# Kernel optimization log

Hardware: AMD Instinct MI355X
Metric: run time of the kernel (lower is better)

Reference implementation:

```python
import jax, jax.numpy as jnp
import numpy as np

H_DIM = 1024
N_HEADS = 16
HEAD_D = H_DIM // N_HEADS  # 64


def setup_inputs() -> dict:
    key = jax.random.key(0)
    ks = jax.random.split(key, 10)
    B, T, C = 2, 2048, H_DIM
    init = 1.0 / np.sqrt(C)  # lecun_normal-scale stand-in
    src = jax.random.normal(ks[0], (B, T, C), dtype=jnp.float32)
    mask = jnp.ones((B, T), dtype=jnp.float32)  # unused when causal
    Wq = jax.random.normal(ks[1], (C, H_DIM), dtype=jnp.float32) * init
    Wk = jax.random.normal(ks[2], (C, H_DIM), dtype=jnp.float32) * init
    Wv = jax.random.normal(ks[3], (C, H_DIM), dtype=jnp.float32) * init
    Wo = jax.random.normal(ks[4], (H_DIM, H_DIM), dtype=jnp.float32) * init
    bq = jnp.zeros((H_DIM,), jnp.float32)
    bk = jnp.zeros((H_DIM,), jnp.float32)
    bv = jnp.zeros((H_DIM,), jnp.float32)
    bo = jnp.zeros((H_DIM,), jnp.float32)
    return {"src": src, "mask": mask, "Wq": Wq, "bq": bq, "Wk": Wk, "bk": bk,
            "Wv": Wv, "bv": bv, "Wo": Wo, "bo": bo}


def reference(src, mask, Wq, bq, Wk, bk, Wv, bv, Wo, bo):
    # MaskedCausalAttention forward, deterministic=True (dropout = identity),
    # use_causal_mask=True.
    B, T, C = src.shape
    N, D = N_HEADS, HEAD_D
    # q,k,v: [B, N, T, D]
    q = (src @ Wq + bq).reshape(B, T, N, D).transpose(0, 2, 1, 3)
    k = (src @ Wk + bk).reshape(B, T, N, D).transpose(0, 2, 1, 3)
    v = (src @ Wv + bv).reshape(B, T, N, D).transpose(0, 2, 1, 3)
    # scores: [B, N, T, T]
    scores = jnp.einsum('bntd,bnsd->bnts', q, k) / jnp.sqrt(jnp.float32(D))
    causal = jnp.tril(jnp.ones((T, T), dtype=bool))[None, None]
    scores = jnp.where(causal, scores, -jnp.inf)
    probs = jax.nn.softmax(scores, axis=-1)
    attn = jnp.einsum('bnts,bnsd->bntd', probs, v)  # [B, N, T, D]
    attn = attn.transpose(0, 2, 1, 3).reshape(B, T, N * D)
    return attn @ Wo + bo
```

## Files before the change

### kernel.cpp

```cpp
#include <hip/hip_runtime.h>
#include <hip/hip_bf16.h>

typedef __hip_bfloat16 bf16;
typedef __attribute__((ext_vector_type(8))) short short8;
typedef __attribute__((ext_vector_type(4))) float f32x4;

#define BATCH 2
#define SEQ   2048
#define HDIM  1024
#define NHEAD 16
#define DHEAD 64
#define MROWS (BATCH*SEQ)

#define QSCALE 0.18033688f
#define EXP2F(x) __builtin_amdgcn_exp2f(x)

static __device__ __forceinline__ short f2bs(float x) {
    __hip_bfloat16 h = (__hip_bfloat16)x;
    return *reinterpret_cast<short*>(&h);
}
static __device__ __forceinline__ unsigned int pk2(float a, float b) {
    __hip_bfloat162 h = __float22bfloat162_rn(make_float2(a, b));
    return *reinterpret_cast<unsigned int*>(&h);
}

static __device__ __forceinline__ void gload16(const void* g, void* l) {
    __builtin_amdgcn_global_load_lds(
        (const __attribute__((address_space(1))) unsigned int*)g,
        (__attribute__((address_space(3))) unsigned int*)l, 16, 0, 0);
}

__global__ __launch_bounds__(256) void prep1(const float* __restrict__ src,
        const float* __restrict__ Wq, const float* __restrict__ Wk,
        const float* __restrict__ Wv, const float* __restrict__ Wo,
        short* __restrict__ Sb, short* __restrict__ WT,
        short* __restrict__ WoT)
{
    __shared__ float t[64][65];
    const int bx = blockIdx.x, tid = threadIdx.x;
    if (bx < 4096) {
        int i = bx * 256 + tid;
        float4 v = ((const float4*)src)[i];
        ushort4 o;
        o.x = (unsigned short)f2bs(v.x);
        o.y = (unsigned short)f2bs(v.y);
        o.z = (unsigned short)f2bs(v.z);
        o.w = (unsigned short)f2bs(v.w);
        ((ushort4*)Sb)[i] = o;
        return;
    }
    const int tb = bx - 4096;
    const int wsel = tb >> 8;
    const float* W = (wsel == 0) ? Wq : (wsel == 1) ? Wk : (wsel == 2) ? Wv : Wo;
    short* dst = (wsel < 3) ? WT : WoT;
    const int roff = (wsel < 3) ? wsel * 1024 : 0;
    const int t8 = tb & 255;
    const int n0 = (t8 & 15) * 64, k0 = (t8 >> 4) * 64;
#pragma unroll
    for (int i = 0; i < 16; i++) {
        int idx = tid + i * 256, r = idx >> 6, c = idx & 63;
        t[r][c] = W[(size_t)(k0 + r) * HDIM + n0 + c];
    }
    __syncthreads();
#pragma unroll
    for (int i = 0; i < 16; i++) {
        int idx = tid + i * 256, c = idx >> 6, r = idx & 63;
        dst[(size_t)(roff + n0 + c) * HDIM + k0 + r] = f2bs(t[r][c]);
    }
}

__global__ __launch_bounds__(512, 2) void gemm_qkv(const short* __restrict__ A,
        const short* __restrict__ Bt,
        const float* __restrict__ bq, const float* __restrict__ bk,
        const float* __restrict__ bv,
        short* __restrict__ Qout, short* __restrict__ Kout,
        short* __restrict__ Vtout)
{
    __shared__ short SM[2][32768];
    const int tid = threadIdx.x, lane = tid & 63, w = tid >> 6;
    const int quad = lane >> 4, l15 = lane & 15;
    const int m0 = blockIdx.y * 256, n0 = blockIdx.x * 256;
    const int wr = w >> 1, wc = w & 1;

    const short* gp[4][2];
    int lo[4][2];
#pragma unroll
    for (int g = 0; g < 4; g++)
#pragma unroll
        for (int i = 0; i < 2; i++) {
            if (g < 2) {
                int u = g * 16 + w * 2 + i;
                gp[g][i] = A + (size_t)(m0 + (u >> 1) * 16 + l15) * HDIM
                             + (u & 1) * 32 + quad * 8;
                lo[g][i] = u * 512;
            } else {
                int j = w * 2 + i;
                int v = (g == 2 ? 0 : 8) + j + (j >= 8 ? 8 : 0);
                gp[g][i] = Bt + (size_t)(n0 + (v >> 1) * 16 + l15) * HDIM
                              + (v & 1) * 32 + quad * 8;
                lo[g][i] = 16384 + v * 512;
            }
        }

    f32x4 acc[4][8];
#pragma unroll
    for (int i = 0; i < 4; i++)
#pragma unroll
        for (int j = 0; j < 8; j++) acc[i][j] = (f32x4){0.f, 0.f, 0.f, 0.f};

#pragma unroll
    for (int g = 0; g < 4; g++)
#pragma unroll
        for (int i = 0; i < 2; i++) { gload16(gp[g][i], &SM[0][lo[g][i]]); gp[g][i] += 64; }
    asm volatile("s_waitcnt vmcnt(2)" ::: "memory");
    __builtin_amdgcn_s_barrier();

    short8 af[4][2];
    for (int t = 0; t < 16; ++t) {
        const short* Tb = SM[t & 1];
        short* Sn = SM[(t + 1) & 1];
#pragma unroll
        for (int p = 0; p < 4; ++p) {
            if (p == 0) {
#pragma unroll
                for (int mi = 0; mi < 4; mi++)
#pragma unroll
                    for (int kh = 0; kh < 2; kh++)
                        af[mi][kh] = *(const short8*)
                            &Tb[((wr * 4 + mi) * 2 + kh) * 512 + lane * 8];
            }
            short8 bfp[2][2];
#pragma unroll
            for (int n2 = 0; n2 < 2; n2++)
#pragma unroll
                for (int kh = 0; kh < 2; kh++)
                    bfp[n2][kh] = *(const short8*)
                        &Tb[16384 + ((wc * 8 + p * 2 + n2) * 2 + kh) * 512 + lane * 8];

            if (t < 15) {
                gload16(gp[p][0], Sn + lo[p][0]); gp[p][0] += 64;
                gload16(gp[p][1], Sn + lo[p][1]); gp[p][1] += 64;
                if (p == 1) asm volatile("s_waitcnt vmcnt(4)" ::: "memory");
                if (p == 3) asm volatile("s_waitcnt vmcnt(2)" ::: "memory");
            } else {
                if (p == 1) asm volatile("s_waitcnt vmcnt(0)" ::: "memory");
            }
            __builtin_amdgcn_s_barrier();
            asm volatile("s_waitcnt lgkmcnt(0)" ::: "memory");
            __builtin_amdgcn_s_setprio(1);
#pragma unroll
            for (int n2 = 0; n2 < 2; n2++)
#pragma unroll
                for (int mi = 0; mi < 4; mi++)
#pragma unroll
                    for (int kh = 0; kh < 2; kh++)
                        acc[mi][p * 2 + n2] = __builtin_amdgcn_mfma_f32_16x16x32_bf16(
                            af[mi][kh], bfp[n2][kh], acc[mi][p * 2 + n2], 0, 0, 0);
            __builtin_amdgcn_s_setprio(0);
            __builtin_amdgcn_s_barrier();
        }
    }

    const int region = blockIdx.x >> 2;
    if (region < 2) {
        const float* bias = region ? bk : bq;
        const float oscale = region ? 1.0f : QSCALE;
        short* C = region ? Kout : Qout;
#pragma unroll
        for (int mi = 0; mi < 4; mi++) {
            int mB = m0 + wr * 64 + mi * 16 + quad * 4;
#pragma unroll
            for (int ni = 0; ni < 8; ni++) {
                int nl = (n0 + (wc * 8 + ni) * 16 + l15) & 1023;
                float bb = bias[nl];
#pragma unroll
                for (int r = 0; r < 4; r++)
                    C[(size_t)(mB + r) * HDIM + nl] =
                        f2bs((acc[mi][ni][r] + bb) * oscale);
            }
        }
    } else {
#pragma unroll
        for (int mi = 0; mi < 4; mi++) {
            int mB = m0 + wr * 64 + mi * 16 + quad * 4;
            int bb = mB >> 11, tt = mB & 2047;
#pragma unroll
            for (int ni = 0; ni < 8; ni++) {
                int n = n0 + (wc * 8 + ni) * 16 + l15;
                int h = (n >> 6) & 15, d = n & 63;
                float bvv = bv[n & 1023];
                size_t base = ((size_t)((bb * NHEAD + h) * DHEAD + d)) * SEQ + tt;
                ushort4 pk;
                pk.x = (unsigned short)f2bs(acc[mi][ni][0] + bvv);
                pk.y = (unsigned short)f2bs(acc[mi][ni][1] + bvv);
                pk.z = (unsigned short)f2bs(acc[mi][ni][2] + bvv);
                pk.w = (unsigned short)f2bs(acc[mi][ni][3] + bvv);
                *(ushort4*)(Vtout + base) = pk;
            }
        }
    }
}

__global__ __launch_bounds__(256) void attn_mfma(const short* __restrict__ Qb,
        const short* __restrict__ Kb, const short* __restrict__ Vt,
        short* __restrict__ Ab)
{
    __shared__ short SMEM[29184];
    const int tid = threadIdx.x, lane = tid & 63, w = tid >> 6;
    const int quad = lane >> 4, l15 = lane & 15;
    const int L = blockIdx.x;

    const int pair = (L & 7) + 8 * ((L >> 3) & 3);
    const int strip = 31 - (L >> 5);
    const int b = pair >> 4, head = pair & 15;

    const short* Kbh = Kb + (size_t)b * SEQ * HDIM + head * DHEAD;
    const short* Vth = Vt + (size_t)(b * NHEAD + head) * DHEAD * SEQ;
    short* Pw = SMEM + 24576 + w * 1152;

    const int qbase = strip * 64;
    const int qr = qbase + w * 16 + l15;

    const short* qptr = Qb + (size_t)(b * SEQ + qr) * HDIM + head * DHEAD + quad * 8;
    short8 bq0 = *(const short8*)qptr;
    short8 bq1 = *(const short8*)(qptr + 32);

    const short* gp[4];
    int stp[4], ldo[4];
#pragma unroll
    for (int i = 0; i < 4; i++) {
        int u = w * 4 + i;
        if (u < 8) {
            int t = u >> 1, h = u & 1;
            gp[i] = Kbh + (size_t)(t * 16 + l15) * HDIM + h * 32 + quad * 8;
            stp[i] = 64 * HDIM;
        } else {
            int c = u - 8, dt = c >> 1, kh = c & 1;
            gp[i] = Vth + (size_t)(dt * 16 + l15) * SEQ + kh * 32 + quad * 8;
            stp[i] = 64;
        }
        ldo[i] = u * 512;
    }

    f32x4 o[4];
#pragma unroll
    for (int dt = 0; dt < 4; dt++) o[dt] = (f32x4){0.f, 0.f, 0.f, 0.f};
    float psum = 0.f;

#pragma unroll
    for (int i = 0; i < 4; i++) { gload16(gp[i], &SMEM[ldo[i]]); gp[i] += stp[i]; }
    if (strip >= 1) {
#pragma unroll
        for (int i = 0; i < 4; i++) { gload16(gp[i], &SMEM[8192 + ldo[i]]); gp[i] += stp[i]; }
    }

    for (int it = 0; it <= strip; ++it) {
        short* Ks = &SMEM[(it % 3) * 8192];
        short* Vs = Ks + 4096;

        if (it + 2 <= strip) {
            short* nb = &SMEM[((it + 2) % 3) * 8192];
#pragma unroll
            for (int i = 0; i < 4; i++) { gload16(gp[i], nb + ldo[i]); gp[i] += stp[i]; }
            asm volatile("s_waitcnt vmcnt(8)" ::: "memory");
        } else if (it + 1 <= strip) {
            asm volatile("s_waitcnt vmcnt(4)" ::: "memory");
        } else {
            asm volatile("s_waitcnt vmcnt(0)" ::: "memory");
        }
        __builtin_amdgcn_s_barrier();
        const int s0 = it * 64;
        f32x4 sv[4];
        __builtin_amdgcn_s_setprio(1);
#pragma unroll
        for (int t = 0; t < 4; t++) {
            sv[t] = (f32x4){0.f, 0.f, 0.f, 0.f};
            short8 k0 = *(const short8*)&Ks[(t * 2) * 512 + lane * 8];
            short8 k1 = *(const short8*)&Ks[(t * 2 + 1) * 512 + lane * 8];
            sv[t] = __builtin_amdgcn_mfma_f32_16x16x32_bf16(k0, bq0, sv[t], 0, 0, 0);
            sv[t] = __builtin_amdgcn_mfma_f32_16x16x32_bf16(k1, bq1, sv[t], 0, 0, 0);
        }
        __builtin_amdgcn_s_setprio(0);

        float p[16];
        if (it == strip) {
#pragma unroll
            for (int t = 0; t < 4; t++)
#pragma unroll
                for (int r = 0; r < 4; r++) {
                    int key = s0 + t * 16 + quad * 4 + r;
                    p[t * 4 + r] = (key <= qr) ? EXP2F(sv[t][r]) : 0.f;
                }
        } else {
#pragma unroll
            for (int t = 0; t < 4; t++)
#pragma unroll
                for (int r = 0; r < 4; r++)
                    p[t * 4 + r] = EXP2F(sv[t][r]);
        }
#pragma unroll
        for (int i = 0; i < 16; i++) psum += p[i];

#pragma unroll
        for (int t = 0; t < 4; t++) {
            uint2 u2;
            u2.x = pk2(p[t * 4],     p[t * 4 + 1]);
            u2.y = pk2(p[t * 4 + 2], p[t * 4 + 3]);
            *(uint2*)&Pw[l15 * 72 + t * 16 + quad * 4] = u2;
        }
        short8 bp0 = *(const short8*)&Pw[l15 * 72 + quad * 8];
        short8 bp1 = *(const short8*)&Pw[l15 * 72 + 32 + quad * 8];

        __builtin_amdgcn_s_setprio(1);
#pragma unroll
        for (int dt = 0; dt < 4; dt++) {
            short8 av0 = *(const short8*)&Vs[(dt * 2) * 512 + lane * 8];
            short8 av1 = *(const short8*)&Vs[(dt * 2 + 1) * 512 + lane * 8];
            o[dt] = __builtin_amdgcn_mfma_f32_16x16x32_bf16(av0, bp0, o[dt], 0, 0, 0);
            o[dt] = __builtin_amdgcn_mfma_f32_16x16x32_bf16(av1, bp1, o[dt], 0, 0, 0);
        }
        __builtin_amdgcn_s_setprio(0);
        __builtin_amdgcn_s_barrier();
    }

    float lrow = psum + __shfl_xor(psum, 16);
    lrow += __shfl_xor(lrow, 32);
    const float inv = 1.f / lrow;

    const size_t obase = (size_t)(b * SEQ + qr) * HDIM + head * DHEAD;
#pragma unroll
    for (int dt = 0; dt < 4; dt++) {
        uint2 u2;
        u2.x = pk2(o[dt][0] * inv, o[dt][1] * inv);
        u2.y = pk2(o[dt][2] * inv, o[dt][3] * inv);
        *(uint2*)&Ab[obase + dt * 16 + quad * 4] = u2;
    }
}

__global__ __launch_bounds__(256) void gemm_o(const short* __restrict__ A,
        const short* __restrict__ Bt, const float* __restrict__ bo,
        float* __restrict__ Out)
{
    __shared__ short SM[3 * 6144];
    const int tid = threadIdx.x, lane = tid & 63, w = tid >> 6;
    const int quad = lane >> 4, l15 = lane & 15;
    const int m0 = blockIdx.y * 64, n0 = blockIdx.x * 128;
    const int wr = w >> 1, wc = w & 1;

    const short* gsrc[3];
    short* ldst[3];
#pragma unroll
    for (int i = 0; i < 3; i++) {
        int u = w * 3 + i;
        if (u < 4) {
            gsrc[i] = A + (size_t)(m0 + u * 16 + l15) * HDIM + quad * 8;
            ldst[i] = &SM[u * 512];
        } else {
            int v = u - 4;
            gsrc[i] = Bt + (size_t)(n0 + v * 16 + l15) * HDIM + quad * 8;
            ldst[i] = &SM[2048 + v * 512];
        }
    }

    f32x4 acc[2][4];
#pragma unroll
    for (int i = 0; i < 2; i++)
#pragma unroll
        for (int j = 0; j < 4; j++) acc[i][j] = (f32x4){0.f, 0.f, 0.f, 0.f};

#pragma unroll
    for (int i = 0; i < 3; i++) { gload16(gsrc[i], ldst[i]); gsrc[i] += 32; }
#pragma unroll
    for (int i = 0; i < 3; i++) { gload16(gsrc[i], ldst[i] + 6144); gsrc[i] += 32; }

    for (int kk = 0; kk < 32; ++kk) {
        if (kk < 30) {
            const int nb = ((kk + 2) % 3) * 6144;
#pragma unroll
            for (int i = 0; i < 3; i++) { gload16(gsrc[i], ldst[i] + nb); gsrc[i] += 32; }
            asm volatile("s_waitcnt vmcnt(6)" ::: "memory");
        } else if (kk == 30) {
            asm volatile("s_waitcnt vmcnt(3)" ::: "memory");
        } else {
            asm volatile("s_waitcnt vmcnt(0)" ::: "memory");
        }
        __builtin_amdgcn_s_barrier();

        const short* Asb = &SM[(kk % 3) * 6144];
        const short* Bsb = Asb + 2048;
        short8 af[2], bfr[4];
#pragma unroll
        for (int mi = 0; mi < 2; mi++)
            af[mi] = *(const short8*)&Asb[(wr * 2 + mi) * 512 + lane * 8];
#pragma unroll
        for (int ni = 0; ni < 4; ni++)
            bfr[ni] = *(const short8*)&Bsb[(wc * 4 + ni) * 512 + lane * 8];
#pragma unroll
        for (int mi = 0; mi < 2; mi++)
#pragma unroll
            for (int ni = 0; ni < 4; ni++)
                acc[mi][ni] = __builtin_amdgcn_mfma_f32_16x16x32_bf16(
                                  af[mi], bfr[ni], acc[mi][ni], 0, 0, 0);
        __builtin_amdgcn_s_barrier();
    }

#pragma unroll
    for (int mi = 0; mi < 2; mi++) {
        int mB = m0 + (wr * 2 + mi) * 16 + quad * 4;
#pragma unroll
        for (int ni = 0; ni < 4; ni++) {
            int n = n0 + (wc * 4 + ni) * 16 + l15;
            float bb = bo[n];
#pragma unroll
            for (int r = 0; r < 4; r++)
                Out[(size_t)(mB + r) * HDIM + n] = acc[mi][ni][r] + bb;
        }
    }
}

extern "C" void kernel_launch(void* const* d_in, const int* in_sizes, int n_in,
                              void* d_out, int out_size, void* d_ws, size_t ws_size,
                              hipStream_t stream)
{
    const float* src = (const float*)d_in[0];
    const float* Wq = (const float*)d_in[2];
    const float* bq = (const float*)d_in[3];
    const float* Wk = (const float*)d_in[4];
    const float* bk = (const float*)d_in[5];
    const float* Wv = (const float*)d_in[6];
    const float* bv = (const float*)d_in[7];
    const float* Wo = (const float*)d_in[8];
    const float* bo = (const float*)d_in[9];
    float* out = (float*)d_out;

    short* Sb   = (short*)d_ws;
    short* Qb   = Sb + (size_t)MROWS * HDIM;
    short* Kb   = Qb + (size_t)MROWS * HDIM;
    short* Vt   = Kb + (size_t)MROWS * HDIM;
    short* WoT  = Vt + (size_t)MROWS * HDIM;
    short* WT   = (short*)d_out;
    short* Ab   = Qb;

    prep1<<<dim3(4096 + 1024), dim3(256), 0, stream>>>(src, Wq, Wk, Wv, Wo, Sb, WT, WoT);

    gemm_qkv<<<dim3(12, 16), dim3(512), 0, stream>>>(Sb, WT, bq, bk, bv, Qb, Kb, Vt);

    attn_mfma<<<dim3(1024), dim3(256), 0, stream>>>(Qb, Kb, Vt, Ab);

    gemm_o<<<dim3(8, 64), dim3(256), 0, stream>>>(Ab, WoT, bo, out);
}
```

Measured before the change: 206.7 us.

## Switch attention and output GEMM to double buffering with larger K tiles

The attention kernel drops from triple to double buffering of K/V tiles, cutting shared memory from about 58KB to 42KB. That should allow more blocks per CU at the cost of a shallower prefetch. The output-projection GEMM now uses a K step of 64 with two buffers instead of 32 with three, halving the iteration and barrier count per block. An explicit lgkmcnt wait after the barrier in the QKV GEMM is also removed, leaving the compiler to insert LDS waits.

After: 203.7 us. No clear change (-1.4%).

```diff
diff --git a/kernel.cpp b/kernel.cpp
--- a/kernel.cpp
+++ b/kernel.cpp
@@ -146,7 +146,6 @@
                 if (p == 1) asm volatile("s_waitcnt vmcnt(0)" ::: "memory");
             }
             __builtin_amdgcn_s_barrier();
-            asm volatile("s_waitcnt lgkmcnt(0)" ::: "memory");
             __builtin_amdgcn_s_setprio(1);
 #pragma unroll
             for (int n2 = 0; n2 < 2; n2++)
@@ -205,7 +204,7 @@
         const short* __restrict__ Kb, const short* __restrict__ Vt,
         short* __restrict__ Ab)
 {
-    __shared__ short SMEM[29184];
+    __shared__ short SMEM[20992];
     const int tid = threadIdx.x, lane = tid & 63, w = tid >> 6;
     const int quad = lane >> 4, l15 = lane & 15;
     const int L = blockIdx.x;
@@ -216,7 +215,7 @@
 
     const short* Kbh = Kb + (size_t)b * SEQ * HDIM + head * DHEAD;
     const short* Vth = Vt + (size_t)(b * NHEAD + head) * DHEAD * SEQ;
-    short* Pw = SMEM + 24576 + w * 1152;
+    short* Pw = SMEM + 16384 + w * 1152;
 
     const int qbase = strip * 64;
     const int qr = qbase + w * 16 + l15;
@@ -249,21 +248,16 @@
 
 #pragma unroll
     for (int i = 0; i < 4; i++) { gload16(gp[i], &SMEM[ldo[i]]); gp[i] += stp[i]; }
-    if (strip >= 1) {
-#pragma unroll
-        for (int i = 0; i < 4; i++) { gload16(gp[i], &SMEM[8192 + ldo[i]]); gp[i] += stp[i]; }
-    }
 
     for (int it = 0; it <= strip; ++it) {
-        short* Ks = &SMEM[(it % 3) * 8192];
+        const int cur = it & 1;
+        short* Ks = &SMEM[cur * 8192];
         short* Vs = Ks + 4096;
 
-        if (it + 2 <= strip) {
-            short* nb = &SMEM[((it + 2) % 3) * 8192];
+        if (it < strip) {
+            short* nb = &SMEM[(cur ^ 1) * 8192];
 #pragma unroll
             for (int i = 0; i < 4; i++) { gload16(gp[i], nb + ldo[i]); gp[i] += stp[i]; }
-            asm volatile("s_waitcnt vmcnt(8)" ::: "memory");
-        } else if (it + 1 <= strip) {
             asm volatile("s_waitcnt vmcnt(4)" ::: "memory");
         } else {
             asm volatile("s_waitcnt vmcnt(0)" ::: "memory");
@@ -341,24 +335,25 @@
         const short* __restrict__ Bt, const float* __restrict__ bo,
         float* __restrict__ Out)
 {
-    __shared__ short SM[3 * 6144];
+    __shared__ short SM[2 * 12288];
     const int tid = threadIdx.x, lane = tid & 63, w = tid >> 6;
     const int quad = lane >> 4, l15 = lane & 15;
     const int m0 = blockIdx.y * 64, n0 = blockIdx.x * 128;
     const int wr = w >> 1, wc = w & 1;
 
-    const short* gsrc[3];
-    short* ldst[3];
-#pragma unroll
-    for (int i = 0; i < 3; i++) {
-        int u = w * 3 + i;
-        if (u < 4) {
-            gsrc[i] = A + (size_t)(m0 + u * 16 + l15) * HDIM + quad * 8;
+    const short* gsrc[6];
+    short* ldst[6];
+#pragma unroll
+    for (int i = 0; i < 6; i++) {
+        int u = w * 6 + i;
+        if (u < 8) {
+            int mi = u >> 1, kh = u & 1;
+            gsrc[i] = A + (size_t)(m0 + mi * 16 + l15) * HDIM + kh * 32 + quad * 8;
             ldst[i] = &SM[u * 512];
         } else {
-            int v = u - 4;
-            gsrc[i] = Bt + (size_t)(n0 + v * 16 + l15) * HDIM + quad * 8;
-            ldst[i] = &SM[2048 + v * 512];
+            int v = u - 8, ni = v >> 1, kh = v & 1;
+            gsrc[i] = Bt + (size_t)(n0 + ni * 16 + l15) * HDIM + kh * 32 + quad * 8;
+            ldst[i] = &SM[4096 + v * 512];
         }
     }
 
@@ -369,38 +364,38 @@
         for (int j = 0; j < 4; j++) acc[i][j] = (f32x4){0.f, 0.f, 0.f, 0.f};
 
 #pragma unroll
-    for (int i = 0; i < 3; i++) { gload16(gsrc[i], ldst[i]); gsrc[i] += 32; }
-#pragma unroll
-    for (int i = 0; i < 3; i++) { gload16(gsrc[i], ldst[i] + 6144); gsrc[i] += 32; }
-
-    for (int kk = 0; kk < 32; ++kk) {
-        if (kk < 30) {
-            const int nb = ((kk + 2) % 3) * 6144;
-#pragma unroll
-            for (int i = 0; i < 3; i++) { gload16(gsrc[i], ldst[i] + nb); gsrc[i] += 32; }
+    for (int i = 0; i < 6; i++) { gload16(gsrc[i], ldst[i]); gsrc[i] += 64; }
+
+    for (int kk = 0; kk < 16; ++kk) {
+        const int cur = kk & 1;
+        if (kk < 15) {
+            const int nb = (cur ^ 1) * 12288;
+#pragma unroll
+            for (int i = 0; i < 6; i++) { gload16(gsrc[i], ldst[i] + nb); gsrc[i] += 64; }
             asm volatile("s_waitcnt vmcnt(6)" ::: "memory");
-        } else if (kk == 30) {
-            asm volatile("s_waitcnt vmcnt(3)" ::: "memory");
         } else {
             asm volatile("s_waitcnt vmcnt(0)" ::: "memory");
         }
         __builtin_amdgcn_s_barrier();
 
-        const short* Asb = &SM[(kk % 3) * 6144];
-        const short* Bsb = Asb + 2048;
-        short8 af[2], bfr[4];
-#pragma unroll
-        for (int mi = 0; mi < 2; mi++)
-            af[mi] = *(const short8*)&Asb[(wr * 2 + mi) * 512 + lane * 8];
-#pragma unroll
-        for (int ni = 0; ni < 4; ni++)
-            bfr[ni] = *(const short8*)&Bsb[(wc * 4 + ni) * 512 + lane * 8];
-#pragma unroll
-        for (int mi = 0; mi < 2; mi++)
+        const short* Asb = &SM[cur * 12288];
+        const short* Bsb = Asb + 4096;
+#pragma unroll
+        for (int kh = 0; kh < 2; kh++) {
+            short8 af[2], bfr[4];
+#pragma unroll
+            for (int mi = 0; mi < 2; mi++)
+                af[mi] = *(const short8*)&Asb[((wr * 2 + mi) * 2 + kh) * 512 + lane * 8];
 #pragma unroll
             for (int ni = 0; ni < 4; ni++)
-                acc[mi][ni] = __builtin_amdgcn_mfma_f32_16x16x32_bf16(
-                                  af[mi], bfr[ni], acc[mi][ni], 0, 0, 0);
+                bfr[ni] = *(const short8*)&Bsb[((wc * 4 + ni) * 2 + kh) * 512 + lane * 8];
+#pragma unroll
+            for (int mi = 0; mi < 2; mi++)
+#pragma unroll
+                for (int ni = 0; ni < 4; ni++)
+                    acc[mi][ni] = __builtin_amdgcn_mfma_f32_16x16x32_bf16(
+                                      af[mi], bfr[ni], acc[mi][ni], 0, 0, 0);
+        }
         __builtin_amdgcn_s_barrier();
     }
 
```
